# Performance work log

Hardware: AMD Instinct MI355X
Metric: run time of the kernel (lower is better)

Reference implementation:

```python
import jax, jax.numpy as jnp
import numpy as np

WIN = 7  # window_size
NUM_HEADS = 8


def _relative_position_index(ws: int) -> np.ndarray:
    # Matches torch.meshgrid default ('ij') indexing used in the module.
    coords = np.stack(np.meshgrid(np.arange(ws), np.arange(ws), indexing='ij'))  # (2, ws, ws)
    flat = coords.reshape(2, -1)                                   # (2, ws*ws)
    rel = flat[:, :, None] - flat[:, None, :]                      # (2, N, N)
    rel = rel.transpose(1, 2, 0).copy()                            # (N, N, 2)
    rel[:, :, 0] += ws - 1
    rel[:, :, 1] += ws - 1
    rel[:, :, 0] *= 2 * ws - 1
    return rel.sum(-1)                                             # (N, N) int


def setup_inputs() -> dict:
    key = jax.random.key(0)
    ks = jax.random.split(key, 7)
    B_, N, C = 4096, WIN * WIN, 256
    nW = 64
    return {
        'x': jax.random.normal(ks[0], (B_, N, C), dtype=jnp.float32),
        'mask': jax.random.normal(ks[1], (nW, N, N), dtype=jnp.float32),
        'qkv_w': jax.random.normal(ks[2], (3 * C, C), dtype=jnp.float32) * 0.02,
        'qkv_b': jax.random.normal(ks[3], (3 * C,), dtype=jnp.float32) * 0.02,
        'proj_w': jax.random.normal(ks[4], (C, C), dtype=jnp.float32) * 0.02,
        'proj_b': jax.random.normal(ks[5], (C,), dtype=jnp.float32) * 0.02,
        'rpb_table': jax.random.normal(ks[6], ((2 * WIN - 1) ** 2, NUM_HEADS), dtype=jnp.float32) * 0.02,
    }


def reference(x, mask, qkv_w, qkv_b, proj_w, proj_b, rpb_table):
    B_, N, C = x.shape
    H = NUM_HEADS
    hd = C // H
    scale = hd ** -0.5
    rpi = jnp.asarray(_relative_position_index(WIN))  # (N, N) int, constant

    qkv = x @ qkv_w.T + qkv_b                          # (B_, N, 3C)
    qkv = qkv.reshape(B_, N, 3, H, hd).transpose(2, 0, 3, 1, 4)  # (3, B_, H, N, hd)
    q, k, v = qkv[0], qkv[1], qkv[2]

    attn = jnp.einsum('bhnd,bhmd->bhnm', q * scale, k)  # (B_, H, N, N)
    bias = rpb_table[rpi.reshape(-1)].reshape(N, N, H).transpose(2, 0, 1)  # (H, N, N)
    attn = attn + bias[None]

    nW = mask.shape[0]
    attn = attn.reshape(B_ // nW, nW, H, N, N) + mask[None, :, None]
    attn = attn.reshape(B_, H, N, N)
    attn = jax.nn.softmax(attn, axis=-1)

    out = jnp.einsum('bhnm,bhmd->bhnd', attn, v)       # (B_, H, N, hd)
    out = out.transpose(0, 2, 1, 3).reshape(B_, N, C)
    return out @ proj_w.T + proj_b
```

## Files before the change

### kernel.cpp

```cpp
#include <hip/hip_runtime.h>

#define SEG 51380224

typedef __attribute__((ext_vector_type(8))) __bf16 bf16x8;
typedef __attribute__((ext_vector_type(4))) __bf16 bf16x4;
typedef __attribute__((ext_vector_type(4))) float f32x4;

static __device__ __forceinline__ bf16x8 bzero8() {
    bf16x8 z;
#pragma unroll
    for (int u = 0; u < 8; ++u) z[u] = (__bf16)0.0f;
    return z;
}

static __device__ __forceinline__ void gl_lds16(const __bf16* g, __bf16* l) {
    __builtin_amdgcn_global_load_lds(
        (const __attribute__((address_space(1))) void*)g,
        (__attribute__((address_space(3))) void*)l, 16, 0, 0);
}

__global__ __launch_bounds__(256)
void cvt_bf16_k(const float* __restrict__ src, __bf16* __restrict__ dst, int n8)
{
    int i = blockIdx.x * 256 + threadIdx.x;
    const int stride = gridDim.x * 256;
    for (; i < n8; i += stride) {
        float4 a = *reinterpret_cast<const float4*>(src + (size_t)i * 8);
        float4 b = *reinterpret_cast<const float4*>(src + (size_t)i * 8 + 4);
        bf16x8 o;
        o[0] = (__bf16)a.x; o[1] = (__bf16)a.y; o[2] = (__bf16)a.z; o[3] = (__bf16)a.w;
        o[4] = (__bf16)b.x; o[5] = (__bf16)b.y; o[6] = (__bf16)b.z; o[7] = (__bf16)b.w;
        *reinterpret_cast<bf16x8*>(dst + (size_t)i * 8) = o;
    }
}

__global__ __launch_bounds__(256)
void expand_add_k(const float* __restrict__ mask, const float* __restrict__ rpb,
                  float* __restrict__ add)
{
    const int wh = blockIdx.x;
    const int w = wh >> 3, h = wh & 7;
    for (int e = threadIdx.x; e < 4096; e += 256) {
        int i = e >> 6, j = e & 63;
        float v = -1e30f;
        if (i < 49 && j < 49) {
            int ih = i / 7, iw = i - ih * 7;
            int jh = j / 7, jw = j - jh * 7;
            int bidx = (ih - jh + 6) * 13 + (iw - jw + 6);
            v = mask[(size_t)w * 2401 + i * 49 + j] + rpb[bidx * 8 + h];
        }
        add[(size_t)wh * 4096 + e] = v;
    }
}

__global__ __launch_bounds__(256)
void qkv_gemm_k(const __bf16* __restrict__ x, const __bf16* __restrict__ w,
                const float* __restrict__ bvec, __bf16* __restrict__ ws)
{
    __shared__ __bf16 As[128][64];
    __shared__ __bf16 Bs[128][64];
    const int tid  = threadIdx.x;
    const int nwg  = 1568 * 6;
    const int bid  = blockIdx.x;
    const int v    = (bid & 7) * (nwg >> 3) + (bid >> 3);
    const int mb   = v / 6, nb = v - mb * 6;
    const int m0   = mb * 128;
    const int n0   = nb * 128;
    const int wave = tid >> 6, lane = tid & 63;
    const int wm   = wave >> 1, wn = wave & 1;
    const int quad = lane >> 4, lm = lane & 15;
    const int koff = quad * 8;

    const int srow = wave * 8 + (lane >> 3);
    const int scol = (lane & 7) * 8;

    f32x4 acc[4][4] = {};

    for (int k0 = 0; k0 < 256; k0 += 64) {
#pragma unroll
        for (int i = 0; i < 4; ++i) {
            int row = i * 32 + srow;
            gl_lds16(x + (size_t)(m0 + row) * 256 + k0 + scol,
                     &As[0][0] + i * 2048 + wave * 512);
            gl_lds16(w + (size_t)(n0 + row) * 256 + k0 + scol,
                     &Bs[0][0] + i * 2048 + wave * 512);
        }
        __syncthreads();
#pragma unroll
        for (int kk = 0; kk < 64; kk += 32) {
            bf16x8 af[4], bfr[4];
#pragma unroll
            for (int mt = 0; mt < 4; ++mt)
                af[mt] = *reinterpret_cast<const bf16x8*>(&As[wm*64 + mt*16 + lm][kk + koff]);
#pragma unroll
            for (int nt = 0; nt < 4; ++nt)
                bfr[nt] = *reinterpret_cast<const bf16x8*>(&Bs[wn*64 + nt*16 + lm][kk + koff]);
#pragma unroll
            for (int mt = 0; mt < 4; ++mt)
#pragma unroll
                for (int nt = 0; nt < 4; ++nt)
                    acc[mt][nt] = __builtin_amdgcn_mfma_f32_16x16x32_bf16(af[mt], bfr[nt], acc[mt][nt], 0, 0, 0);
        }
        __syncthreads();
    }

#pragma unroll
    for (int nt = 0; nt < 4; ++nt) {
        int j  = n0 + wn*64 + nt*16 + lm;
        int c3 = j >> 8, hh = (j >> 5) & 7, d = j & 31;
        float bj  = bvec[j];
        float scl = (c3 == 0) ? 0.17677669529663687f : 1.0f;
#pragma unroll
        for (int mt = 0; mt < 4; ++mt)
#pragma unroll
            for (int r = 0; r < 4; ++r) {
                int m = m0 + wm*64 + mt*16 + quad*4 + r;
                int b = m / 49, nw = m - b * 49;
                float vv = (acc[mt][nt][r] + bj) * scl;
                ws[(size_t)c3 * SEG + ((size_t)((b*8 + hh)*49 + nw))*32 + d] = (__bf16)vv;
            }
    }
}

__global__ __launch_bounds__(64)
void attn_mfma_k(const __bf16* __restrict__ ws, const float* __restrict__ add,
                 __bf16* __restrict__ pre)
{
    __shared__ __bf16 Pl[64 * 72];
    __shared__ __bf16 Vt[32 * 72];
    const int lane = threadIdx.x;
    const int bh   = blockIdx.x;
    const int b    = bh >> 3, h = bh & 7;
    const int wh   = ((b & 63) << 3) | h;
    const int quad = lane >> 4, lm = lane & 15;
    const int koff = quad * 8;

    const __bf16* qp = ws + (size_t)bh * (49 * 32);
    const __bf16* kp = qp + SEG;
    const __bf16* vp = qp + (size_t)2 * SEG;

    {
        int d = lane >> 1, j0 = 48 + (lane & 1) * 8;
        *reinterpret_cast<bf16x8*>(&Vt[d * 72 + j0]) = bzero8();
    }
#pragma unroll
    for (int t = 0; t < 4; ++t) {
        int idx = lane + t * 64;
        if (idx < 196) {
            int j = idx >> 2, c8 = (idx & 3) * 8;
            bf16x8 vv = *reinterpret_cast<const bf16x8*>(vp + j * 32 + c8);
#pragma unroll
            for (int u = 0; u < 8; ++u) Vt[(c8 + u) * 72 + j] = vv[u];
        }
    }

    bf16x8 qf[4], kf[4];
#pragma unroll
    for (int t = 0; t < 4; ++t)
        qf[t] = *reinterpret_cast<const bf16x8*>(qp + (t * 16 + lm) * 32 + koff);
#pragma unroll
    for (int t = 0; t < 4; ++t) {
        int m = t * 16 + lm;
        kf[t] = (m < 49) ? *reinterpret_cast<const bf16x8*>(kp + m * 32 + koff)
                         : bzero8();
    }

    f32x4 s[4][4] = {};
#pragma unroll
    for (int mt = 0; mt < 4; ++mt)
#pragma unroll
        for (int nt = 0; nt < 4; ++nt)
            s[mt][nt] = __builtin_amdgcn_mfma_f32_16x16x32_bf16(kf[mt], qf[nt], s[mt][nt], 0, 0, 0);

    const float* ap = add + (size_t)wh * 4096;
#pragma unroll
    for (int nt = 0; nt < 4; ++nt) {
        int i = nt * 16 + lm;
#pragma unroll
        for (int mt = 0; mt < 4; ++mt) {
            f32x4 a4 = *reinterpret_cast<const f32x4*>(ap + i * 64 + mt * 16 + quad * 4);
            s[mt][nt] += a4;
        }
    }

#pragma unroll
    for (int nt = 0; nt < 4; ++nt) {
        float mx = -3.0e38f;
#pragma unroll
        for (int mt = 0; mt < 4; ++mt)
#pragma unroll
            for (int r = 0; r < 4; ++r) mx = fmaxf(mx, s[mt][nt][r]);
        mx = fmaxf(mx, __shfl_xor(mx, 16));
        mx = fmaxf(mx, __shfl_xor(mx, 32));
        float sum = 0.f;
#pragma unroll
        for (int mt = 0; mt < 4; ++mt)
#pragma unroll
            for (int r = 0; r < 4; ++r) {
                float e = __expf(s[mt][nt][r] - mx);
                s[mt][nt][r] = e; sum += e;
            }
        sum += __shfl_xor(sum, 16);
        sum += __shfl_xor(sum, 32);
        float rl = 1.0f / sum;
#pragma unroll
        for (int mt = 0; mt < 4; ++mt)
#pragma unroll
            for (int r = 0; r < 4; ++r) s[mt][nt][r] *= rl;
    }

#pragma unroll
    for (int nt = 0; nt < 4; ++nt) {
        int i = nt * 16 + lm;
#pragma unroll
        for (int mt = 0; mt < 4; ++mt) {
            bf16x4 p4;
#pragma unroll
            for (int r = 0; r < 4; ++r) p4[r] = (__bf16)s[mt][nt][r];
            *reinterpret_cast<bf16x4*>(&Pl[i * 72 + mt * 16 + quad * 4]) = p4;
        }
    }
    __syncthreads();

    f32x4 o[4][2] = {};
#pragma unroll
    for (int kt = 0; kt < 2; ++kt) {
        bf16x8 vf[2];
#pragma unroll
        for (int dt = 0; dt < 2; ++dt)
            vf[dt] = *reinterpret_cast<const bf16x8*>(&Vt[(dt * 16 + lm) * 72 + kt * 32 + koff]);
#pragma unroll
        for (int mt2 = 0; mt2 < 4; ++mt2) {
            bf16x8 pf = *reinterpret_cast<const bf16x8*>(&Pl[(mt2 * 16 + lm) * 72 + kt * 32 + koff]);
#pragma unroll
            for (int dt = 0; dt < 2; ++dt)
                o[mt2][dt] = __builtin_amdgcn_mfma_f32_16x16x32_bf16(pf, vf[dt], o[mt2][dt], 0, 0, 0);
        }
    }

#pragma unroll
    for (int mt2 = 0; mt2 < 4; ++mt2) {
        int ib = mt2 * 16 + quad * 4;
#pragma unroll
        for (int r = 0; r < 4; ++r) {
            int i = ib + r;
            if (i < 49) {
                size_t base = ((size_t)(b * 49 + i)) * 256 + h * 32;
                pre[base + lm]      = (__bf16)o[mt2][0][r];
                pre[base + 16 + lm] = (__bf16)o[mt2][1][r];
            }
        }
    }
}

__global__ __launch_bounds__(256)
void proj_gemm_k(const __bf16* __restrict__ pre, const __bf16* __restrict__ w,
                 const float* __restrict__ bvec, float* __restrict__ out)
{
    __shared__ __bf16 As[128][64];
    __shared__ __bf16 Bs[128][64];
    const int tid  = threadIdx.x;
    const int nwg  = 1568 * 2;
    const int bid  = blockIdx.x;
    const int v    = (bid & 7) * (nwg >> 3) + (bid >> 3);
    const int mb   = v >> 1, nb = v & 1;
    const int m0   = mb * 128;
    const int n0   = nb * 128;
    const int wave = tid >> 6, lane = tid & 63;
    const int wm   = wave >> 1, wn = wave & 1;
    const int quad = lane >> 4, lm = lane & 15;
    const int koff = quad * 8;

    const int srow = wave * 8 + (lane >> 3);
    const int scol = (lane & 7) * 8;

    f32x4 acc[4][4] = {};

    for (int k0 = 0; k0 < 256; k0 += 64) {
#pragma unroll
        for (int i = 0; i < 4; ++i) {
            int row = i * 32 + srow;
            gl_lds16(pre + (size_t)(m0 + row) * 256 + k0 + scol,
                     &As[0][0] + i * 2048 + wave * 512);
            gl_lds16(w + (size_t)(n0 + row) * 256 + k0 + scol,
                     &Bs[0][0] + i * 2048 + wave * 512);
        }
        __syncthreads();
#pragma unroll
        for (int kk = 0; kk < 64; kk += 32) {
            bf16x8 af[4], bfr[4];
#pragma unroll
            for (int mt = 0; mt < 4; ++mt)
                af[mt] = *reinterpret_cast<const bf16x8*>(&As[wm*64 + mt*16 + lm][kk + koff]);
#pragma unroll
            for (int nt = 0; nt < 4; ++nt)
                bfr[nt] = *reinterpret_cast<const bf16x8*>(&Bs[wn*64 + nt*16 + lm][kk + koff]);
#pragma unroll
            for (int mt = 0; mt < 4; ++mt)
#pragma unroll
                for (int nt = 0; nt < 4; ++nt)
                    acc[mt][nt] = __builtin_amdgcn_mfma_f32_16x16x32_bf16(af[mt], bfr[nt], acc[mt][nt], 0, 0, 0);
        }
        __syncthreads();
    }

#pragma unroll
    for (int nt = 0; nt < 4; ++nt) {
        int j = n0 + wn*64 + nt*16 + lm;
        float bj = bvec[j];
#pragma unroll
        for (int mt = 0; mt < 4; ++mt)
#pragma unroll
            for (int r = 0; r < 4; ++r) {
                int m = m0 + wm*64 + mt*16 + quad*4 + r;
                out[(size_t)m*256 + j] = acc[mt][nt][r] + bj;
            }
    }
}

extern "C" void kernel_launch(void* const* d_in, const int* in_sizes, int n_in,
                              void* d_out, int out_size, void* d_ws, size_t ws_size,
                              hipStream_t stream)
{
    const float* x      = (const float*)d_in[0];
    const float* mask   = (const float*)d_in[1];
    const float* qkv_w  = (const float*)d_in[2];
    const float* qkv_b  = (const float*)d_in[3];
    const float* proj_w = (const float*)d_in[4];
    const float* proj_b = (const float*)d_in[5];
    const float* rpb    = (const float*)d_in[6];

    __bf16* ws  = (__bf16*)d_ws;
    __bf16* pre = ws + (size_t)3 * SEG;
    float*  out = (float*)d_out;

    char*   ob      = (char*)d_out;
    float*  addbuf  = (float*)ob;
    __bf16* qkv_wb  = (__bf16*)(ob + (10u << 20));
    __bf16* xb      = (__bf16*)(ob + (16u << 20));
    __bf16* proj_wb = ws;

    cvt_bf16_k<<<dim3(2048), 256, 0, stream>>>(x, xb, 51380224 / 8);
    cvt_bf16_k<<<dim3(96),   256, 0, stream>>>(qkv_w, qkv_wb, 196608 / 8);
    expand_add_k<<<dim3(512), 256, 0, stream>>>(mask, rpb, addbuf);
    qkv_gemm_k<<<dim3(1568 * 6), 256, 0, stream>>>(xb, qkv_wb, qkv_b, ws);
    attn_mfma_k<<<dim3(32768), 64, 0, stream>>>(ws, addbuf, pre);
    cvt_bf16_k<<<dim3(32),   256, 0, stream>>>(proj_w, proj_wb, 65536 / 8);
    proj_gemm_k<<<dim3(1568 * 2), 256, 0, stream>>>(pre, proj_wb, proj_b, out);
}
```

Before: 782.6 us.

## Double-buffer LDS tiles with XOR swizzle in QKV and projection GEMMs

Both GEMM kernels now keep two LDS buffers per operand and issue the next K-tile's global-to-LDS loads before computing the current tile, so load latency overlaps MFMA work. Staging columns are XOR-swizzled by row to cut LDS bank conflicts on the fragment reads, and s_setprio raises wave priority during the MFMA loop. This doubles LDS use per block to 64KB, which can lower occupancy. The K loop is only four steps, so the overlap window is short.

```diff
diff --git a/kernel.cpp b/kernel.cpp
--- a/kernel.cpp
+++ b/kernel.cpp
@@ -57,8 +57,8 @@
 void qkv_gemm_k(const __bf16* __restrict__ x, const __bf16* __restrict__ w,
                 const float* __restrict__ bvec, __bf16* __restrict__ ws)
 {
-    __shared__ __bf16 As[128][64];
-    __shared__ __bf16 Bs[128][64];
+    __shared__ __bf16 As[2][128][64];
+    __shared__ __bf16 Bs[2][128][64];
     const int tid  = threadIdx.x;
     const int nwg  = 1568 * 6;
     const int bid  = blockIdx.x;
@@ -69,39 +69,63 @@
     const int wave = tid >> 6, lane = tid & 63;
     const int wm   = wave >> 1, wn = wave & 1;
     const int quad = lane >> 4, lm = lane & 15;
-    const int koff = quad * 8;
 
     const int srow = wave * 8 + (lane >> 3);
-    const int scol = (lane & 7) * 8;
+    const int scol = (((lane & 7) ^ (lane >> 3)) << 3);
 
     f32x4 acc[4][4] = {};
 
-    for (int k0 = 0; k0 < 256; k0 += 64) {
-#pragma unroll
-        for (int i = 0; i < 4; ++i) {
-            int row = i * 32 + srow;
-            gl_lds16(x + (size_t)(m0 + row) * 256 + k0 + scol,
-                     &As[0][0] + i * 2048 + wave * 512);
-            gl_lds16(w + (size_t)(n0 + row) * 256 + k0 + scol,
-                     &Bs[0][0] + i * 2048 + wave * 512);
-        }
-        __syncthreads();
+#pragma unroll
+    for (int i = 0; i < 4; ++i) {
+        int row = i * 32 + srow;
+        gl_lds16(x + (size_t)(m0 + row) * 256 + 0 + scol,
+                 &As[0][0][0] + i * 2048 + wave * 512);
+        gl_lds16(w + (size_t)(n0 + row) * 256 + 0 + scol,
+                 &Bs[0][0][0] + i * 2048 + wave * 512);
+    }
+    asm volatile("s_waitcnt vmcnt(0)" ::: "memory");
+    __builtin_amdgcn_s_barrier();
+
+#pragma unroll
+    for (int t = 0; t < 4; ++t) {
+        if (t < 3) {
+            const int k0 = (t + 1) * 64;
+            const int nb2 = (t + 1) & 1;
+#pragma unroll
+            for (int i = 0; i < 4; ++i) {
+                int row = i * 32 + srow;
+                gl_lds16(x + (size_t)(m0 + row) * 256 + k0 + scol,
+                         &As[nb2][0][0] + i * 2048 + wave * 512);
+                gl_lds16(w + (size_t)(n0 + row) * 256 + k0 + scol,
+                         &Bs[nb2][0][0] + i * 2048 + wave * 512);
+            }
+        }
+        const __bf16* Ab = &As[t & 1][0][0];
+        const __bf16* Bb = &Bs[t & 1][0][0];
+        __builtin_amdgcn_s_setprio(1);
 #pragma unroll
         for (int kk = 0; kk < 64; kk += 32) {
+            const int cl = (kk >> 3) + quad;
             bf16x8 af[4], bfr[4];
 #pragma unroll
-            for (int mt = 0; mt < 4; ++mt)
-                af[mt] = *reinterpret_cast<const bf16x8*>(&As[wm*64 + mt*16 + lm][kk + koff]);
-#pragma unroll
-            for (int nt = 0; nt < 4; ++nt)
-                bfr[nt] = *reinterpret_cast<const bf16x8*>(&Bs[wn*64 + nt*16 + lm][kk + koff]);
+            for (int mt = 0; mt < 4; ++mt) {
+                int row = wm * 64 + mt * 16 + lm;
+                af[mt] = *reinterpret_cast<const bf16x8*>(Ab + row * 64 + ((cl ^ (lm & 7)) << 3));
+            }
+#pragma unroll
+            for (int nt = 0; nt < 4; ++nt) {
+                int row = wn * 64 + nt * 16 + lm;
+                bfr[nt] = *reinterpret_cast<const bf16x8*>(Bb + row * 64 + ((cl ^ (lm & 7)) << 3));
+            }
 #pragma unroll
             for (int mt = 0; mt < 4; ++mt)
 #pragma unroll
                 for (int nt = 0; nt < 4; ++nt)
                     acc[mt][nt] = __builtin_amdgcn_mfma_f32_16x16x32_bf16(af[mt], bfr[nt], acc[mt][nt], 0, 0, 0);
         }
-        __syncthreads();
+        __builtin_amdgcn_s_setprio(0);
+        asm volatile("s_waitcnt vmcnt(0)" ::: "memory");
+        __builtin_amdgcn_s_barrier();
     }
 
 #pragma unroll
@@ -257,8 +281,8 @@
 void proj_gemm_k(const __bf16* __restrict__ pre, const __bf16* __restrict__ w,
                  const float* __restrict__ bvec, float* __restrict__ out)
 {
-    __shared__ __bf16 As[128][64];
-    __shared__ __bf16 Bs[128][64];
+    __shared__ __bf16 As[2][128][64];
+    __shared__ __bf16 Bs[2][128][64];
     const int tid  = threadIdx.x;
     const int nwg  = 1568 * 2;
     const int bid  = blockIdx.x;
@@ -269,39 +293,63 @@
     const int wave = tid >> 6, lane = tid & 63;
     const int wm   = wave >> 1, wn = wave & 1;
     const int quad = lane >> 4, lm = lane & 15;
-    const int koff = quad * 8;
 
     const int srow = wave * 8 + (lane >> 3);
-    const int scol = (lane & 7) * 8;
+    const int scol = (((lane & 7) ^ (lane >> 3)) << 3);
 
     f32x4 acc[4][4] = {};
 
-    for (int k0 = 0; k0 < 256; k0 += 64) {
-#pragma unroll
-        for (int i = 0; i < 4; ++i) {
-            int row = i * 32 + srow;
-            gl_lds16(pre + (size_t)(m0 + row) * 256 + k0 + scol,
-                     &As[0][0] + i * 2048 + wave * 512);
-            gl_lds16(w + (size_t)(n0 + row) * 256 + k0 + scol,
-                     &Bs[0][0] + i * 2048 + wave * 512);
-        }
-        __syncthreads();
+#pragma unroll
+    for (int i = 0; i < 4; ++i) {
+        int row = i * 32 + srow;
+        gl_lds16(pre + (size_t)(m0 + row) * 256 + 0 + scol,
+                 &As[0][0][0] + i * 2048 + wave * 512);
+        gl_lds16(w + (size_t)(n0 + row) * 256 + 0 + scol,
+                 &Bs[0][0][0] + i * 2048 + wave * 512);
+    }
+    asm volatile("s_waitcnt vmcnt(0)" ::: "memory");
+    __builtin_amdgcn_s_barrier();
+
+#pragma unroll
+    for (int t = 0; t < 4; ++t) {
+        if (t < 3) {
+            const int k0 = (t + 1) * 64;
+            const int nb2 = (t + 1) & 1;
+#pragma unroll
+            for (int i = 0; i < 4; ++i) {
+                int row = i * 32 + srow;
+                gl_lds16(pre + (size_t)(m0 + row) * 256 + k0 + scol,
+                         &As[nb2][0][0] + i * 2048 + wave * 512);
+                gl_lds16(w + (size_t)(n0 + row) * 256 + k0 + scol,
+                         &Bs[nb2][0][0] + i * 2048 + wave * 512);
+            }
+        }
+        const __bf16* Ab = &As[t & 1][0][0];
+        const __bf16* Bb = &Bs[t & 1][0][0];
+        __builtin_amdgcn_s_setprio(1);
 #pragma unroll
         for (int kk = 0; kk < 64; kk += 32) {
+            const int cl = (kk >> 3) + quad;
             bf16x8 af[4], bfr[4];
 #pragma unroll
-            for (int mt = 0; mt < 4; ++mt)
-                af[mt] = *reinterpret_cast<const bf16x8*>(&As[wm*64 + mt*16 + lm][kk + koff]);
-#pragma unroll
-            for (int nt = 0; nt < 4; ++nt)
-                bfr[nt] = *reinterpret_cast<const bf16x8*>(&Bs[wn*64 + nt*16 + lm][kk + koff]);
+            for (int mt = 0; mt < 4; ++mt) {
+                int row = wm * 64 + mt * 16 + lm;
+                af[mt] = *reinterpret_cast<const bf16x8*>(Ab + row * 64 + ((cl ^ (lm & 7)) << 3));
+            }
+#pragma unroll
+            for (int nt = 0; nt < 4; ++nt) {
+                int row = wn * 64 + nt * 16 + lm;
+                bfr[nt] = *reinterpret_cast<const bf16x8*>(Bb + row * 64 + ((cl ^ (lm & 7)) << 3));
+            }
 #pragma unroll
             for (int mt = 0; mt < 4; ++mt)
 #pragma unroll
                 for (int nt = 0; nt < 4; ++nt)
                     acc[mt][nt] = __builtin_amdgcn_mfma_f32_16x16x32_bf16(af[mt], bfr[nt], acc[mt][nt], 0, 0, 0);
         }
-        __syncthreads();
+        __builtin_amdgcn_s_setprio(0);
+        asm volatile("s_waitcnt vmcnt(0)" ::: "memory");
+        __builtin_amdgcn_s_barrier();
     }
 
 #pragma unroll
```

Result: no change. 788.1 us (+0.7%).
